# Kernel tuning notes

Hardware: AMD Instinct MI355X
Metric: run time of the kernel (lower is better)

## Reference

```python
import jax, jax.numpy as jnp
import numpy as np

B = 16384
SIZES = [512, 256, 256, 128]  # layer_sizes, layer 0 = clamped input
K = 16        # settling iterations
ETA = 0.1     # eta_x, scale 'none' => effective eta per layer = 0.1
CLIP = 1.0    # dx_clip


def setup_inputs() -> dict:
    key = jax.random.key(0)
    k0, k1, k2, k3 = jax.random.split(key, 4)
    x0 = jax.random.normal(k0, (B, SIZES[0]), jnp.float32)
    # W[l]: (D_{l+1}, D_l), init scale 1/sqrt(D_{l+1}) as in torch code
    W0 = jax.random.normal(k1, (SIZES[1], SIZES[0]), jnp.float32) * (1.0 / np.sqrt(SIZES[1]))
    W1 = jax.random.normal(k2, (SIZES[2], SIZES[1]), jnp.float32) * (1.0 / np.sqrt(SIZES[2]))
    W2 = jax.random.normal(k3, (SIZES[3], SIZES[2]), jnp.float32) * (1.0 / np.sqrt(SIZES[3]))
    return {"x0": x0, "W0": W0, "W1": W1, "W2": W2}


def _f(z):
    return jnp.tanh(z)


def _f_prime(z):
    t = jnp.tanh(z)
    return 1.0 - t * t


def _settle(x0, Ws):
    """Run K settling steps. Layer 0 clamped to x0; layers 1..L free."""
    L = len(Ws)
    bsz = x0.shape[0]
    xs0 = (x0,) + tuple(jnp.zeros((bsz, w.shape[0]), x0.dtype) for w in Ws)

    def step(xs, _):
        xs = list(xs)
        # top-down predictions: preact[l] = x[l+1] @ W[l], shape (B, D_l)
        preacts = [xs[l + 1] @ Ws[l] for l in range(L)]
        errs = [xs[l] - _f(preacts[l]) for l in range(L)]
        new = [xs[0]]  # layer 0 clamped
        for l in range(1, L + 1):
            # feedback: (e[l-1] * f'(preact[l-1])) @ W[l-1].T  (tied weights)
            dx = (errs[l - 1] * _f_prime(preacts[l - 1])) @ Ws[l - 1].T
            if l < L:
                dx = dx - errs[l]
            dx = jnp.clip(dx, -CLIP, CLIP)
            new.append(xs[l] + ETA * dx)
        return tuple(new), None

    final, _ = jax.lax.scan(step, xs0, None, length=K)
    return final


def reference(x0, W0, W1, W2):
    final = _settle(x0, (W0, W1, W2))
    # return settled latent (layer L) state, shape (B, 128)
    return final[-1]
```

## Files before the change

kernel.cpp:

```cpp
#include <hip/hip_runtime.h>

typedef _Float16 half8 __attribute__((ext_vector_type(8)));
typedef float floatx4 __attribute__((ext_vector_type(4)));

#define DEV_INLINE __device__ __forceinline__

constexpr int D0 = 512, D1 = 256, D2 = 256, D3 = 128;
constexpr int NROWS = 16384;
constexpr int MBLK = 32;
constexpr int NBLK = NROWS / MBLK;
constexpr int KITERS = 16;
constexpr float ETA = 0.1f;

constexpr int OFF_WF0 = 0;
constexpr int OFF_WF1 = OFF_WF0 + D1 * D0;
constexpr int OFF_WF2 = OFF_WF1 + D2 * D1;
constexpr int OFF_WB0 = OFF_WF2 + D3 * D2;
constexpr int OFF_WB1 = OFF_WB0 + D0 * D1;
constexpr int OFF_WB2 = OFF_WB1 + D1 * D2;
constexpr int PACK_ELEMS = OFF_WB2 + D2 * D3;

__global__ void repack_kernel(const float* __restrict__ W0, const float* __restrict__ W1,
                              const float* __restrict__ W2, const float* __restrict__ x0,
                              _Float16* __restrict__ pack, _Float16* __restrict__ x0h,
                              int do_x0) {
  int p = blockIdx.x * 256 + threadIdx.x;
  if (p < PACK_ELEMS) {
    const float* W; int Csrc, Nd, off; bool tr;
    if (p < OFF_WF1)      { W = W0; Csrc = D0; Nd = D0; off = OFF_WF0; tr = false; }
    else if (p < OFF_WF2) { W = W1; Csrc = D1; Nd = D1; off = OFF_WF1; tr = false; }
    else if (p < OFF_WB0) { W = W2; Csrc = D2; Nd = D2; off = OFF_WF2; tr = false; }
    else if (p < OFF_WB1) { W = W0; Csrc = D0; Nd = D1; off = OFF_WB0; tr = true;  }
    else if (p < OFF_WB2) { W = W1; Csrc = D1; Nd = D1; off = OFF_WB1; tr = true;  }
    else                  { W = W2; Csrc = D2; Nd = D3; off = OFF_WB2; tr = true;  }
    int local = p - off;
    int j  = local & 7;
    int l  = (local >> 3) & 63;
    int fr = local >> 9;
    int NT = Nd >> 4;
    int nt = fr % NT, kt = fr / NT;
    int k = kt * 32 + ((l >> 4) << 3) + j;
    int n = nt * 16 + (l & 15);
    float v = tr ? W[n * Csrc + k] : W[k * Csrc + n];
    pack[p] = (_Float16)v;
  } else if (do_x0) {
    int q = p - PACK_ELEMS;
    if (q < NROWS * D0) x0h[q] = (_Float16)x0[q];
  }
}

DEV_INLINE float fast_tanh(float x) {
  float e = __expf(2.f * x);
  return 1.f - 2.f * __builtin_amdgcn_rcpf(e + 1.f);
}

DEV_INLINE const _Float16* bpt(const _Float16* Bp, int nt, int lane) {
  return Bp + ((size_t)nt * 64 + lane) * 8;
}

template <int RT, int KSTEPS, int CT, int NTT, int STRB, int AS>
DEV_INLINE void mm_burst(const char* __restrict__ A, const _Float16* __restrict__ bsrc,
                         int lane, floatx4* acc) {
  static_assert(KSTEPS * CT <= 8, "bq register budget");
  const int arow = lane & 15;
  const int aoff = (lane >> 4) << 4;
  half8 bq[KSTEPS * CT];
#pragma unroll
  for (int s = 0; s < KSTEPS; ++s)
#pragma unroll
    for (int ct = 0; ct < CT; ++ct)
      bq[s * CT + ct] = *(const half8*)(bsrc + (size_t)(s * NTT + ct) * 512);
#pragma unroll
  for (int k0 = 0; k0 < KSTEPS; ++k0) {
    half8 a[RT];
#pragma unroll
    for (int rt = 0; rt < RT; ++rt) {
      int row = rt * 16 + arow;
      int byte = (row * STRB + k0 * 64 + aoff) ^ ((row & 7) << 4);
      a[rt] = *(const half8*)(A + byte);
    }
#pragma unroll
    for (int ct = 0; ct < CT; ++ct)
#pragma unroll
      for (int rt = 0; rt < RT; ++rt)
        acc[rt * AS + ct] =
            __builtin_amdgcn_mfma_f32_16x16x32_f16(a[rt], bq[k0 * CT + ct], acc[rt * AS + ct], 0, 0, 0);
  }
}

__global__ __launch_bounds__(512)
void settle_kernel(const float* __restrict__ x0,
                   const _Float16* __restrict__ x0h,
                   const _Float16* __restrict__ pack,
                   float* __restrict__ out) {
  extern __shared__ char lds[];
  char* AX1 = lds;
  char* AG0 = lds + 16384;
  char* AQ  = lds + 24576;
  char* AG1 = lds + 40960;
  char* AR  = lds + 57344;

  const int tid  = threadIdx.x;
  const int lane = tid & 63;
  const int wave = tid >> 6;
  const int row0 = blockIdx.x * MBLK;
  const int rsub = (lane >> 4) << 2;
  const int csub = lane & 15;

  {
    floatx4 z = {0.f, 0.f, 0.f, 0.f};
    for (int i = tid; i < 1024; i += 512) ((floatx4*)AQ)[i] = z;
    for (int i = tid; i < 512; i += 512) ((floatx4*)AR)[i] = z;
  }

  const floatx4 zf = {0.f, 0.f, 0.f, 0.f};
  floatx4 x3m[2];
#pragma unroll
  for (int i = 0; i < 2; ++i) x3m[i] = zf;

  const _Float16* Wf0 = pack + OFF_WF0;
  const _Float16* Wf1 = pack + OFF_WF1;
  const _Float16* Wf2 = pack + OFF_WF2;
  const _Float16* Wb0 = pack + OFF_WB0;
  const _Float16* Wb1 = pack + OFF_WB1;
  const _Float16* Wb2 = pack + OFF_WB2;

  {
    floatx4 dx1a[4];
#pragma unroll
    for (int i = 0; i < 4; ++i) dx1a[i] = zf;
    for (int q = 0; q < 4; ++q) {
      for (int idx = tid; idx < MBLK * 128; idx += 512) {
        int row = idx >> 7, colq = idx & 127;
        size_t gi = (size_t)(row0 + row) * D0 + q * 128 + colq;
        _Float16 v = x0h ? x0h[gi] : (_Float16)x0[gi];
        int byte = (row * 256 + colq * 2) ^ ((row & 7) << 4);
        *(_Float16*)(AG0 + byte) = v;
      }
      __syncthreads();
      mm_burst<2, 4, 2, 16, 256, 2>(AG0, bpt(Wb0 + q * 32768, wave * 2, lane), lane, dx1a);
      __syncthreads();
    }
#pragma unroll
    for (int rt = 0; rt < 2; ++rt)
#pragma unroll
      for (int ct = 0; ct < 2; ++ct) {
        int col = (wave * 2 + ct) * 16 + csub;
#pragma unroll
        for (int i = 0; i < 4; ++i) {
          int row = rt * 16 + rsub + i;
          float dx = fminf(1.f, fmaxf(-1.f, dx1a[rt * 2 + ct][i]));
          int byte = (row * 512 + col * 2) ^ ((row & 7) << 4);
          *(_Float16*)(AX1 + byte) = (_Float16)(ETA * dx);
        }
      }
    __syncthreads();
  }

  for (int it = 1; it < KITERS; ++it) {
    floatx4 dx1a[4];
    {
#pragma unroll
      for (int i = 0; i < 4; ++i) dx1a[i] = zf;
#pragma unroll
      for (int ct = 0; ct < 2; ++ct)
        mm_burst<2, 8, 1, 16, 512, 2>(AQ, bpt(Wf1, wave * 2 + ct, lane), lane, &dx1a[ct]);
#pragma unroll
      for (int rt = 0; rt < 2; ++rt)
#pragma unroll
        for (int ct = 0; ct < 2; ++ct) {
          int col = (wave * 2 + ct) * 16 + csub;
#pragma unroll
          for (int i = 0; i < 4; ++i) {
            int row = rt * 16 + rsub + i;
            int sb = (row * 512 + col * 2) ^ ((row & 7) << 4);
            float t = fast_tanh(dx1a[rt * 2 + ct][i]);
            float x1o = (float)*(const _Float16*)(AX1 + sb);
            float e = x1o - t;
            *(_Float16*)(AG1 + sb) = (_Float16)(e * (1.f - t * t));
            dx1a[rt * 2 + ct][i] = -e;
          }
        }
    }
    for (int q = 0; q < 4; ++q) {
      {
        floatx4 acc3[2];
#pragma unroll
        for (int i = 0; i < 2; ++i) acc3[i] = zf;
        mm_burst<2, 8, 1, 32, 512, 1>(AX1, bpt(Wf0, q * 8 + wave, lane), lane, acc3);
        int colq = wave * 16 + csub;
#pragma unroll
        for (int rt = 0; rt < 2; ++rt)
#pragma unroll
          for (int i = 0; i < 4; ++i) {
            int row = rt * 16 + rsub + i;
            float t = fast_tanh(acc3[rt][i]);
            size_t gi = (size_t)(row0 + row) * D0 + q * 128 + colq;
            float xv = x0h ? (float)x0h[gi] : x0[gi];
            float g = (xv - t) * (1.f - t * t);
            int byte = (row * 256 + colq * 2) ^ ((row & 7) << 4);
            *(_Float16*)(AG0 + byte) = (_Float16)g;
          }
      }
      __syncthreads();
      mm_burst<2, 4, 2, 16, 256, 2>(AG0, bpt(Wb0 + q * 32768, wave * 2, lane), lane, dx1a);
      __syncthreads();
    }
#pragma unroll
    for (int rt = 0; rt < 2; ++rt)
#pragma unroll
      for (int ct = 0; ct < 2; ++ct) {
        int col = (wave * 2 + ct) * 16 + csub;
#pragma unroll
        for (int i = 0; i < 4; ++i) {
          int row = rt * 16 + rsub + i;
          int sb = (row * 512 + col * 2) ^ ((row & 7) << 4);
          float dx = fminf(1.f, fmaxf(-1.f, dx1a[rt * 2 + ct][i]));
          float x1o = (float)*(const _Float16*)(AX1 + sb);
          *(_Float16*)(AX1 + sb) = (_Float16)(x1o + ETA * dx);
        }
      }
    floatx4 dx2a[4];
    half8 g2h[2];
    {
      floatx4 p2[4];
#pragma unroll
      for (int i = 0; i < 4; ++i) p2[i] = zf;
      mm_burst<2, 4, 2, 16, 256, 2>(AR, bpt(Wf2, wave * 2, lane), lane, p2);
#pragma unroll
      for (int rt = 0; rt < 2; ++rt)
#pragma unroll
        for (int ct = 0; ct < 2; ++ct) {
          int col = (wave * 2 + ct) * 16 + csub;
#pragma unroll
          for (int i = 0; i < 4; ++i) {
            int row = rt * 16 + rsub + i;
            int sb = (row * 512 + col * 2) ^ ((row & 7) << 4);
            float t = fast_tanh(p2[rt * 2 + ct][i]);
            float x2o = (float)*(const _Float16*)(AQ + sb);
            float e = x2o - t;
            int li = (rt * 2 + ct) * 4 + i;
            g2h[li >> 3][li & 7] = (_Float16)(e * (1.f - t * t));
            dx2a[rt * 2 + ct][i] = -e;
          }
        }
    }
    {
#pragma unroll
      for (int ct = 0; ct < 2; ++ct)
        mm_burst<2, 8, 1, 16, 512, 2>(AG1, bpt(Wb1, wave * 2 + ct, lane), lane, &dx2a[ct]);
#pragma unroll
      for (int rt = 0; rt < 2; ++rt)
#pragma unroll
        for (int ct = 0; ct < 2; ++ct) {
          int col = (wave * 2 + ct) * 16 + csub;
#pragma unroll
          for (int i = 0; i < 4; ++i) {
            int row = rt * 16 + rsub + i;
            int sb = (row * 512 + col * 2) ^ ((row & 7) << 4);
            float dx = fminf(1.f, fmaxf(-1.f, dx2a[rt * 2 + ct][i]));
            float x2o = (float)*(const _Float16*)(AQ + sb);
            *(_Float16*)(AQ + sb) = (_Float16)(x2o + ETA * dx);
          }
        }
    }
    __syncthreads();
#pragma unroll
    for (int rt = 0; rt < 2; ++rt)
#pragma unroll
      for (int ct = 0; ct < 2; ++ct) {
        int col = (wave * 2 + ct) * 16 + csub;
#pragma unroll
        for (int i = 0; i < 4; ++i) {
          int row = rt * 16 + rsub + i;
          int sb = (row * 512 + col * 2) ^ ((row & 7) << 4);
          int li = (rt * 2 + ct) * 4 + i;
          *(_Float16*)(AG1 + sb) = g2h[li >> 3][li & 7];
        }
      }
    __syncthreads();
    {
      floatx4 acc6[2];
#pragma unroll
      for (int i = 0; i < 2; ++i) acc6[i] = zf;
      mm_burst<2, 8, 1, 8, 512, 1>(AG1, bpt(Wb2, wave, lane), lane, acc6);
      __syncthreads();
      int col = wave * 16 + csub;
#pragma unroll
      for (int rt = 0; rt < 2; ++rt)
#pragma unroll
        for (int i = 0; i < 4; ++i) {
          int row = rt * 16 + rsub + i;
          float dx = fminf(1.f, fmaxf(-1.f, acc6[rt][i]));
          float nv = x3m[rt][i] + ETA * dx;
          x3m[rt][i] = nv;
          int byte = (row * 256 + col * 2) ^ ((row & 7) << 4);
          *(_Float16*)(AR + byte) = (_Float16)nv;
        }
    }
  }

  {
    int col = wave * 16 + csub;
#pragma unroll
    for (int rt = 0; rt < 2; ++rt)
#pragma unroll
      for (int i = 0; i < 4; ++i) {
        int row = rt * 16 + rsub + i;
        out[(size_t)(row0 + row) * D3 + col] = x3m[rt][i];
      }
  }
}

extern "C" void kernel_launch(void* const* d_in, const int* in_sizes, int n_in,
                              void* d_out, int out_size, void* d_ws, size_t ws_size,
                              hipStream_t stream) {
  const float* x0 = (const float*)d_in[0];
  const float* W0 = (const float*)d_in[1];
  const float* W1 = (const float*)d_in[2];
  const float* W2 = (const float*)d_in[3];
  float* out = (float*)d_out;

  _Float16* pack = (_Float16*)d_ws;
  const size_t pack_bytes = (size_t)PACK_ELEMS * 2;
  const size_t x0h_bytes = (size_t)NROWS * D0 * 2;
  int do_x0 = (ws_size >= pack_bytes + x0h_bytes) ? 1 : 0;
  _Float16* x0h = do_x0 ? (_Float16*)((char*)d_ws + pack_bytes) : nullptr;

  int total = PACK_ELEMS + (do_x0 ? NROWS * D0 : 0);
  repack_kernel<<<(total + 255) / 256, 256, 0, stream>>>(W0, W1, W2, x0, pack, x0h, do_x0);

  (void)hipFuncSetAttribute(reinterpret_cast<const void*>(settle_kernel),
                            hipFuncAttributeMaxDynamicSharedMemorySize, 65536);
  settle_kernel<<<NBLK, 512, 65536, stream>>>(x0, x0h, pack, out);
}
```

Baseline: 991.3 us.

## Double-buffer weight fragment loads across GEMM stages in registers

Splits the fused load-and-multiply helper into separate weight-fragment load and MFMA compute steps. Two register buffers alternate so the global weight loads for the next GEMM stage are issued before the current stage's MFMAs, hiding global-memory latency across the settle loop. It also replaces __syncthreads with a barrier that waits only on LDS counters, so outstanding global prefetches are not drained at each barrier. The cost is 16 extra half8 registers per lane held live, which raises register pressure and may lower occupancy.

```diff
diff --git a/kernel.cpp b/kernel.cpp
--- a/kernel.cpp
+++ b/kernel.cpp
@@ -58,20 +58,30 @@
   return Bp + ((size_t)nt * 64 + lane) * 8;
 }
 
-template <int RT, int KSTEPS, int CT, int NTT, int STRB, int AS>
-DEV_INLINE void mm_burst(const char* __restrict__ A, const _Float16* __restrict__ bsrc,
-                         int lane, floatx4* acc) {
-  static_assert(KSTEPS * CT <= 8, "bq register budget");
+DEV_INLINE void lds_barrier() {
+  asm volatile("s_waitcnt lgkmcnt(0)" ::: "memory");
+  __builtin_amdgcn_sched_barrier(0);
+  __builtin_amdgcn_s_barrier();
+  __builtin_amdgcn_sched_barrier(0);
+}
+
+template <int KS, int CT, int NTT>
+DEV_INLINE void bq_load(half8* __restrict__ v, const _Float16* __restrict__ bsrc) {
+  static_assert(KS * CT <= 8, "bq register budget");
+#pragma unroll
+  for (int s = 0; s < KS; ++s)
+#pragma unroll
+    for (int ct = 0; ct < CT; ++ct)
+      v[s * CT + ct] = *(const half8*)(bsrc + (size_t)(s * NTT + ct) * 512);
+}
+
+template <int RT, int KS, int CT, int STRB, int AS>
+DEV_INLINE void bq_compute(const char* __restrict__ A, const half8* __restrict__ v,
+                           int lane, floatx4* acc) {
   const int arow = lane & 15;
   const int aoff = (lane >> 4) << 4;
-  half8 bq[KSTEPS * CT];
-#pragma unroll
-  for (int s = 0; s < KSTEPS; ++s)
-#pragma unroll
-    for (int ct = 0; ct < CT; ++ct)
-      bq[s * CT + ct] = *(const half8*)(bsrc + (size_t)(s * NTT + ct) * 512);
-#pragma unroll
-  for (int k0 = 0; k0 < KSTEPS; ++k0) {
+#pragma unroll
+  for (int k0 = 0; k0 < KS; ++k0) {
     half8 a[RT];
 #pragma unroll
     for (int rt = 0; rt < RT; ++rt) {
@@ -84,7 +94,7 @@
 #pragma unroll
       for (int rt = 0; rt < RT; ++rt)
         acc[rt * AS + ct] =
-            __builtin_amdgcn_mfma_f32_16x16x32_f16(a[rt], bq[k0 * CT + ct], acc[rt * AS + ct], 0, 0, 0);
+            __builtin_amdgcn_mfma_f32_16x16x32_f16(a[rt], v[k0 * CT + ct], acc[rt * AS + ct], 0, 0, 0);
   }
 }
 
@@ -125,11 +135,14 @@
   const _Float16* Wb1 = pack + OFF_WB1;
   const _Float16* Wb2 = pack + OFF_WB2;
 
+  half8 bqA[8], bqB[8];
+
   {
     floatx4 dx1a[4];
 #pragma unroll
     for (int i = 0; i < 4; ++i) dx1a[i] = zf;
     for (int q = 0; q < 4; ++q) {
+      bq_load<4, 2, 16>(bqA, bpt(Wb0 + q * 32768, wave * 2, lane));
       for (int idx = tid; idx < MBLK * 128; idx += 512) {
         int row = idx >> 7, colq = idx & 127;
         size_t gi = (size_t)(row0 + row) * D0 + q * 128 + colq;
@@ -137,9 +150,9 @@
         int byte = (row * 256 + colq * 2) ^ ((row & 7) << 4);
         *(_Float16*)(AG0 + byte) = v;
       }
-      __syncthreads();
-      mm_burst<2, 4, 2, 16, 256, 2>(AG0, bpt(Wb0 + q * 32768, wave * 2, lane), lane, dx1a);
-      __syncthreads();
+      lds_barrier();
+      bq_compute<2, 4, 2, 256, 2>(AG0, bqA, lane, dx1a);
+      lds_barrier();
     }
 #pragma unroll
     for (int rt = 0; rt < 2; ++rt)
@@ -154,40 +167,42 @@
           *(_Float16*)(AX1 + byte) = (_Float16)(ETA * dx);
         }
       }
-    __syncthreads();
-  }
+    lds_barrier();
+  }
+
+  bq_load<8, 1, 16>(bqA, bpt(Wf1, wave * 2, lane));
 
   for (int it = 1; it < KITERS; ++it) {
     floatx4 dx1a[4];
-    {
-#pragma unroll
-      for (int i = 0; i < 4; ++i) dx1a[i] = zf;
-#pragma unroll
-      for (int ct = 0; ct < 2; ++ct)
-        mm_burst<2, 8, 1, 16, 512, 2>(AQ, bpt(Wf1, wave * 2 + ct, lane), lane, &dx1a[ct]);
-#pragma unroll
-      for (int rt = 0; rt < 2; ++rt)
-#pragma unroll
-        for (int ct = 0; ct < 2; ++ct) {
-          int col = (wave * 2 + ct) * 16 + csub;
-#pragma unroll
-          for (int i = 0; i < 4; ++i) {
-            int row = rt * 16 + rsub + i;
-            int sb = (row * 512 + col * 2) ^ ((row & 7) << 4);
-            float t = fast_tanh(dx1a[rt * 2 + ct][i]);
-            float x1o = (float)*(const _Float16*)(AX1 + sb);
-            float e = x1o - t;
-            *(_Float16*)(AG1 + sb) = (_Float16)(e * (1.f - t * t));
-            dx1a[rt * 2 + ct][i] = -e;
-          }
-        }
-    }
+    bq_load<8, 1, 16>(bqB, bpt(Wf1, wave * 2 + 1, lane));
+#pragma unroll
+    for (int i = 0; i < 4; ++i) dx1a[i] = zf;
+    bq_compute<2, 8, 1, 512, 2>(AQ, bqA, lane, &dx1a[0]);
+    bq_load<8, 1, 32>(bqA, bpt(Wf0, wave, lane));
+    bq_compute<2, 8, 1, 512, 2>(AQ, bqB, lane, &dx1a[1]);
+#pragma unroll
+    for (int rt = 0; rt < 2; ++rt)
+#pragma unroll
+      for (int ct = 0; ct < 2; ++ct) {
+        int col = (wave * 2 + ct) * 16 + csub;
+#pragma unroll
+        for (int i = 0; i < 4; ++i) {
+          int row = rt * 16 + rsub + i;
+          int sb = (row * 512 + col * 2) ^ ((row & 7) << 4);
+          float t = fast_tanh(dx1a[rt * 2 + ct][i]);
+          float x1o = (float)*(const _Float16*)(AX1 + sb);
+          float e = x1o - t;
+          *(_Float16*)(AG1 + sb) = (_Float16)(e * (1.f - t * t));
+          dx1a[rt * 2 + ct][i] = -e;
+        }
+      }
     for (int q = 0; q < 4; ++q) {
+      bq_load<4, 2, 16>(bqB, bpt(Wb0 + q * 32768, wave * 2, lane));
       {
         floatx4 acc3[2];
 #pragma unroll
         for (int i = 0; i < 2; ++i) acc3[i] = zf;
-        mm_burst<2, 8, 1, 32, 512, 1>(AX1, bpt(Wf0, q * 8 + wave, lane), lane, acc3);
+        bq_compute<2, 8, 1, 512, 1>(AX1, bqA, lane, acc3);
         int colq = wave * 16 + csub;
 #pragma unroll
         for (int rt = 0; rt < 2; ++rt)
@@ -202,9 +217,11 @@
             *(_Float16*)(AG0 + byte) = (_Float16)g;
           }
       }
-      __syncthreads();
-      mm_burst<2, 4, 2, 16, 256, 2>(AG0, bpt(Wb0 + q * 32768, wave * 2, lane), lane, dx1a);
-      __syncthreads();
+      lds_barrier();
+      if (q < 3) bq_load<8, 1, 32>(bqA, bpt(Wf0, (q + 1) * 8 + wave, lane));
+      else       bq_load<4, 2, 16>(bqA, bpt(Wf2, wave * 2, lane));
+      bq_compute<2, 4, 2, 256, 2>(AG0, bqB, lane, dx1a);
+      lds_barrier();
     }
 #pragma unroll
     for (int rt = 0; rt < 2; ++rt)
@@ -223,10 +240,11 @@
     floatx4 dx2a[4];
     half8 g2h[2];
     {
+      bq_load<8, 1, 16>(bqB, bpt(Wb1, wave * 2, lane));
       floatx4 p2[4];
 #pragma unroll
       for (int i = 0; i < 4; ++i) p2[i] = zf;
-      mm_burst<2, 4, 2, 16, 256, 2>(AR, bpt(Wf2, wave * 2, lane), lane, p2);
+      bq_compute<2, 4, 2, 256, 2>(AR, bqA, lane, p2);
 #pragma unroll
       for (int rt = 0; rt < 2; ++rt)
 #pragma unroll
@@ -245,26 +263,25 @@
           }
         }
     }
-    {
-#pragma unroll
-      for (int ct = 0; ct < 2; ++ct)
-        mm_burst<2, 8, 1, 16, 512, 2>(AG1, bpt(Wb1, wave * 2 + ct, lane), lane, &dx2a[ct]);
-#pragma unroll
-      for (int rt = 0; rt < 2; ++rt)
-#pragma unroll
-        for (int ct = 0; ct < 2; ++ct) {
-          int col = (wave * 2 + ct) * 16 + csub;
-#pragma unroll
-          for (int i = 0; i < 4; ++i) {
-            int row = rt * 16 + rsub + i;
-            int sb = (row * 512 + col * 2) ^ ((row & 7) << 4);
-            float dx = fminf(1.f, fmaxf(-1.f, dx2a[rt * 2 + ct][i]));
-            float x2o = (float)*(const _Float16*)(AQ + sb);
-            *(_Float16*)(AQ + sb) = (_Float16)(x2o + ETA * dx);
-          }
-        }
-    }
-    __syncthreads();
+    bq_load<8, 1, 16>(bqA, bpt(Wb1, wave * 2 + 1, lane));
+    bq_compute<2, 8, 1, 512, 2>(AG1, bqB, lane, &dx2a[0]);
+    bq_load<8, 1, 8>(bqB, bpt(Wb2, wave, lane));
+    bq_compute<2, 8, 1, 512, 2>(AG1, bqA, lane, &dx2a[1]);
+#pragma unroll
+    for (int rt = 0; rt < 2; ++rt)
+#pragma unroll
+      for (int ct = 0; ct < 2; ++ct) {
+        int col = (wave * 2 + ct) * 16 + csub;
+#pragma unroll
+        for (int i = 0; i < 4; ++i) {
+          int row = rt * 16 + rsub + i;
+          int sb = (row * 512 + col * 2) ^ ((row & 7) << 4);
+          float dx = fminf(1.f, fmaxf(-1.f, dx2a[rt * 2 + ct][i]));
+          float x2o = (float)*(const _Float16*)(AQ + sb);
+          *(_Float16*)(AQ + sb) = (_Float16)(x2o + ETA * dx);
+        }
+      }
+    lds_barrier();
 #pragma unroll
     for (int rt = 0; rt < 2; ++rt)
 #pragma unroll
@@ -278,13 +295,14 @@
           *(_Float16*)(AG1 + sb) = g2h[li >> 3][li & 7];
         }
       }
-    __syncthreads();
+    lds_barrier();
     {
+      bq_load<8, 1, 16>(bqA, bpt(Wf1, wave * 2, lane));
       floatx4 acc6[2];
 #pragma unroll
       for (int i = 0; i < 2; ++i) acc6[i] = zf;
-      mm_burst<2, 8, 1, 8, 512, 1>(AG1, bpt(Wb2, wave, lane), lane, acc6);
-      __syncthreads();
+      bq_compute<2, 8, 1, 512, 1>(AG1, bqB, lane, acc6);
+      lds_barrier();
       int col = wave * 16 + csub;
 #pragma unroll
       for (int rt = 0; rt < 2; ++rt)
```

Measured after the change: 1.195 ms. 1.21x slower.

## Stage x0 tile in LDS once per block instead of reloading from global

Applied to the files above, without the earlier changes.

Each block now loads its 32x512 tile of x0 into a new 32KB swizzled LDS region as fp16 at kernel start. The first feedback matmul reads it directly, without per-quarter global staging and barriers. The per-iteration error computation reads x0 from LDS rather than global memory. The global fp16 x0 conversion pass in the repack kernel is removed. Dynamic shared memory rises from 64KB to 96KB, which may reduce how many blocks fit per CU.

```diff
diff --git a/kernel.cpp b/kernel.cpp
--- a/kernel.cpp
+++ b/kernel.cpp
@@ -21,32 +21,26 @@
 constexpr int PACK_ELEMS = OFF_WB2 + D2 * D3;
 
 __global__ void repack_kernel(const float* __restrict__ W0, const float* __restrict__ W1,
-                              const float* __restrict__ W2, const float* __restrict__ x0,
-                              _Float16* __restrict__ pack, _Float16* __restrict__ x0h,
-                              int do_x0) {
+                              const float* __restrict__ W2, _Float16* __restrict__ pack) {
   int p = blockIdx.x * 256 + threadIdx.x;
-  if (p < PACK_ELEMS) {
-    const float* W; int Csrc, Nd, off; bool tr;
-    if (p < OFF_WF1)      { W = W0; Csrc = D0; Nd = D0; off = OFF_WF0; tr = false; }
-    else if (p < OFF_WF2) { W = W1; Csrc = D1; Nd = D1; off = OFF_WF1; tr = false; }
-    else if (p < OFF_WB0) { W = W2; Csrc = D2; Nd = D2; off = OFF_WF2; tr = false; }
-    else if (p < OFF_WB1) { W = W0; Csrc = D0; Nd = D1; off = OFF_WB0; tr = true;  }
-    else if (p < OFF_WB2) { W = W1; Csrc = D1; Nd = D1; off = OFF_WB1; tr = true;  }
-    else                  { W = W2; Csrc = D2; Nd = D3; off = OFF_WB2; tr = true;  }
-    int local = p - off;
-    int j  = local & 7;
-    int l  = (local >> 3) & 63;
-    int fr = local >> 9;
-    int NT = Nd >> 4;
-    int nt = fr % NT, kt = fr / NT;
-    int k = kt * 32 + ((l >> 4) << 3) + j;
-    int n = nt * 16 + (l & 15);
-    float v = tr ? W[n * Csrc + k] : W[k * Csrc + n];
-    pack[p] = (_Float16)v;
-  } else if (do_x0) {
-    int q = p - PACK_ELEMS;
-    if (q < NROWS * D0) x0h[q] = (_Float16)x0[q];
-  }
+  if (p >= PACK_ELEMS) return;
+  const float* W; int Csrc, Nd, off; bool tr;
+  if (p < OFF_WF1)      { W = W0; Csrc = D0; Nd = D0; off = OFF_WF0; tr = false; }
+  else if (p < OFF_WF2) { W = W1; Csrc = D1; Nd = D1; off = OFF_WF1; tr = false; }
+  else if (p < OFF_WB0) { W = W2; Csrc = D2; Nd = D2; off = OFF_WF2; tr = false; }
+  else if (p < OFF_WB1) { W = W0; Csrc = D0; Nd = D1; off = OFF_WB0; tr = true;  }
+  else if (p < OFF_WB2) { W = W1; Csrc = D1; Nd = D1; off = OFF_WB1; tr = true;  }
+  else                  { W = W2; Csrc = D2; Nd = D3; off = OFF_WB2; tr = true;  }
+  int local = p - off;
+  int j  = local & 7;
+  int l  = (local >> 3) & 63;
+  int fr = local >> 9;
+  int NT = Nd >> 4;
+  int nt = fr % NT, kt = fr / NT;
+  int k = kt * 32 + ((l >> 4) << 3) + j;
+  int n = nt * 16 + (l & 15);
+  float v = tr ? W[n * Csrc + k] : W[k * Csrc + n];
+  pack[p] = (_Float16)v;
 }
 
 DEV_INLINE float fast_tanh(float x) {
@@ -90,7 +84,6 @@
 
 __global__ __launch_bounds__(512)
 void settle_kernel(const float* __restrict__ x0,
-                   const _Float16* __restrict__ x0h,
                    const _Float16* __restrict__ pack,
                    float* __restrict__ out) {
   extern __shared__ char lds[];
@@ -99,6 +92,7 @@
   char* AQ  = lds + 24576;
   char* AG1 = lds + 40960;
   char* AR  = lds + 57344;
+  char* AX0 = lds + 65536;
 
   const int tid  = threadIdx.x;
   const int lane = tid & 63;
@@ -108,10 +102,17 @@
   const int csub = lane & 15;
 
   {
+    for (int idx = tid; idx < MBLK * D0; idx += 512) {
+      int row = idx >> 9, col = idx & 511;
+      _Float16 v = (_Float16)x0[(size_t)(row0 + row) * D0 + col];
+      int byte = (row * 1024 + col * 2) ^ ((row & 7) << 4);
+      *(_Float16*)(AX0 + byte) = v;
+    }
     floatx4 z = {0.f, 0.f, 0.f, 0.f};
     for (int i = tid; i < 1024; i += 512) ((floatx4*)AQ)[i] = z;
     for (int i = tid; i < 512; i += 512) ((floatx4*)AR)[i] = z;
   }
+  __syncthreads();
 
   const floatx4 zf = {0.f, 0.f, 0.f, 0.f};
   floatx4 x3m[2];
@@ -129,18 +130,10 @@
     floatx4 dx1a[4];
 #pragma unroll
     for (int i = 0; i < 4; ++i) dx1a[i] = zf;
-    for (int q = 0; q < 4; ++q) {
-      for (int idx = tid; idx < MBLK * 128; idx += 512) {
-        int row = idx >> 7, colq = idx & 127;
-        size_t gi = (size_t)(row0 + row) * D0 + q * 128 + colq;
-        _Float16 v = x0h ? x0h[gi] : (_Float16)x0[gi];
-        int byte = (row * 256 + colq * 2) ^ ((row & 7) << 4);
-        *(_Float16*)(AG0 + byte) = v;
-      }
-      __syncthreads();
-      mm_burst<2, 4, 2, 16, 256, 2>(AG0, bpt(Wb0 + q * 32768, wave * 2, lane), lane, dx1a);
-      __syncthreads();
-    }
+#pragma unroll
+    for (int q = 0; q < 4; ++q)
+      mm_burst<2, 4, 2, 16, 1024, 2>(AX0 + q * 256, bpt(Wb0 + q * 32768, wave * 2, lane),
+                                     lane, dx1a);
 #pragma unroll
     for (int rt = 0; rt < 2; ++rt)
 #pragma unroll
@@ -195,8 +188,8 @@
           for (int i = 0; i < 4; ++i) {
             int row = rt * 16 + rsub + i;
             float t = fast_tanh(acc3[rt][i]);
-            size_t gi = (size_t)(row0 + row) * D0 + q * 128 + colq;
-            float xv = x0h ? (float)x0h[gi] : x0[gi];
+            int xb = (row * 1024 + (q * 128 + colq) * 2) ^ ((row & 7) << 4);
+            float xv = (float)*(const _Float16*)(AX0 + xb);
             float g = (xv - t) * (1.f - t * t);
             int byte = (row * 256 + colq * 2) ^ ((row & 7) << 4);
             *(_Float16*)(AG0 + byte) = (_Float16)g;
@@ -322,15 +315,9 @@
   float* out = (float*)d_out;
 
   _Float16* pack = (_Float16*)d_ws;
-  const size_t pack_bytes = (size_t)PACK_ELEMS * 2;
-  const size_t x0h_bytes = (size_t)NROWS * D0 * 2;
-  int do_x0 = (ws_size >= pack_bytes + x0h_bytes) ? 1 : 0;
-  _Float16* x0h = do_x0 ? (_Float16*)((char*)d_ws + pack_bytes) : nullptr;
-
-  int total = PACK_ELEMS + (do_x0 ? NROWS * D0 : 0);
-  repack_kernel<<<(total + 255) / 256, 256, 0, stream>>>(W0, W1, W2, x0, pack, x0h, do_x0);
+  repack_kernel<<<(PACK_ELEMS + 255) / 256, 256, 0, stream>>>(W0, W1, W2, pack);
 
   (void)hipFuncSetAttribute(reinterpret_cast<const void*>(settle_kernel),
-                            hipFuncAttributeMaxDynamicSharedMemorySize, 65536);
-  settle_kernel<<<NBLK, 512, 65536, stream>>>(x0, x0h, pack, out);
-}
+                            hipFuncAttributeMaxDynamicSharedMemorySize, 98304);
+  settle_kernel<<<NBLK, 512, 98304, stream>>>(x0, pack, out);
+}
```

Result: slower. 1.208 ms (+21.9%).
